# Performance work log

Hardware: AMD Instinct MI355X
Metric: run time of the kernel (lower is better)

The kernel has to match this reference:

```python
import jax, jax.numpy as jnp
import numpy as np

B, S, K, H = 512, 128, 4, 128  # batch, seq_len, interest_num, hidden_size
ROUTING_TIMES = 3
EPS = 1e-9


def setup_inputs() -> dict:
    key = jax.random.key(0)
    k1, k2 = jax.random.split(key)
    item_eb = jax.random.normal(k1, (B, S, H), dtype=jnp.float32)
    mask = jnp.ones((B, S), dtype=jnp.float32)
    # learned bilinear map parameter (bilinear_type == 2)
    w = jax.random.normal(k2, (1, S, K * H, H), dtype=jnp.float32) * 0.02
    return {"item_eb": item_eb, "mask": mask, "w": w}


def _squash(cap):
    # cap: [B, K, 1, H]
    n = jnp.sum(cap * cap, axis=-1, keepdims=True)
    return (n / (1.0 + n) / jnp.sqrt(n + EPS)) * cap


def reference(item_eb, mask, w):
    # bilinear_type==2: sum(w[:, :S] * item_eb[:, :, None, :], axis=3)
    # expressed as an einsum to avoid the [B,S,K*H,H] intermediate
    item_eb_hat = jnp.einsum('bsh,sdh->bsd', item_eb, w[0])          # [B, S, K*H]
    item_eb_hat = item_eb_hat.reshape(B, S, K, H).transpose(0, 2, 1, 3)  # [B, K, S, H]
    hat_iter = jax.lax.stop_gradient(item_eb_hat)  # stop_grad=True

    atten_mask = jnp.broadcast_to(mask[:, None, :], (B, K, S))
    capsule_weight = jnp.zeros((B, K, S), dtype=item_eb.dtype)  # bilinear_type > 0

    interest_capsule = None
    for i in range(ROUTING_TIMES):
        # torch F.softmax with implicit dim on a 3D tensor -> dim=0 (legacy)
        sw = jax.nn.softmax(capsule_weight, axis=0)
        sw = jnp.where(atten_mask == 0, 0.0, sw)[:, :, None, :]  # [B, K, 1, S]
        src = hat_iter if i < 2 else item_eb_hat
        interest_capsule = _squash(jnp.matmul(sw, src))  # [B, K, 1, H]
        if i < 2:
            delta = jnp.matmul(hat_iter, interest_capsule.transpose(0, 1, 3, 2))  # [B,K,S,1]
            capsule_weight = capsule_weight + delta.reshape(B, K, S)

    return interest_capsule.reshape(B, K, H)
```

## Files before the change

### kernel.cpp

```cpp
#include <hip/hip_runtime.h>
#include <math.h>

#define BB 512
#define SS 128
#define KK 4
#define HH 128
#define DD 512

typedef __attribute__((ext_vector_type(8))) short bf16x8;
typedef __attribute__((ext_vector_type(4))) float f32x4;

__device__ __forceinline__ unsigned short f2bf(float f) {
  unsigned u = __float_as_uint(f);
  unsigned r = u + 0x7fffu + ((u >> 16) & 1u);
  return (unsigned short)(r >> 16);
}
__device__ __forceinline__ ushort4 f2bf4(float4 v) {
  ushort4 o; o.x = f2bf(v.x); o.y = f2bf(v.y); o.z = f2bf(v.z); o.w = f2bf(v.w);
  return o;
}
__device__ __forceinline__ float bfhi(unsigned u) { return __uint_as_float(u & 0xffff0000u); }
__device__ __forceinline__ float bflo(unsigned u) { return __uint_as_float(u << 16); }

__global__ __launch_bounds__(256) void einsum_mfma(
    const float* __restrict__ item,
    const float* __restrict__ w,
    unsigned short* __restrict__ hat)
{
  __shared__ unsigned short Al[128 * 128];
  __shared__ unsigned short Wl[2][128 * 64];
  const int s  = blockIdx.x;
  const int b0 = blockIdx.y * 128;
  const int t  = threadIdx.x;
  const int lane = t & 63, wvq = t >> 6;
  const int qm = wvq & 1, qn = wvq >> 1;
  const int n16 = lane & 15, kq = lane >> 4;

  const float* Abase = item + ((size_t)b0 * SS + s) * HH;
  const float* Wbase = w + (size_t)s * DD * HH;

  const int ac = t & 31, ar0 = t >> 5;
  const int wc = t & 15, wr0 = t >> 4;
  float4 apre[16];
  #pragma unroll
  for (int j = 0; j < 16; ++j)
    apre[j] = *(const float4*)(Abase + (size_t)(ar0 + 8 * j) * (SS * HH) + ac * 4);
  float4 wpre[8];
  #pragma unroll
  for (int j = 0; j < 8; ++j)
    wpre[j] = *(const float4*)(Wbase + (size_t)(wr0 + 16 * j) * HH + wc * 4);

  #pragma unroll
  for (int j = 0; j < 16; ++j) {
    const int r = ar0 + 8 * j;
    const int lg = ac >> 1;
    *(ushort4*)&Al[r * 128 + ((lg ^ (r & 15)) * 8) + (ac & 1) * 4] = f2bf4(apre[j]);
  }
  #pragma unroll
  for (int j = 0; j < 8; ++j) {
    const int r = wr0 + 16 * j;
    *(ushort4*)&Wl[0][r * 64 + ((((wc >> 1) + r) & 7) * 8) + (wc & 1) * 4] = f2bf4(wpre[j]);
  }
  __syncthreads();

  int buf = 0;
  for (int dt = 0; dt < 4; ++dt) {
    f32x4 acc[4][4] = {};
    #pragma unroll
    for (int hs = 0; hs < 2; ++hs) {
      const int step = dt * 2 + hs;
      if (step < 7) {
        const int d0n = ((step + 1) >> 1) * 128;
        const int ksn = ((step + 1) & 1) * 64;
        #pragma unroll
        for (int j = 0; j < 8; ++j)
          wpre[j] = *(const float4*)(Wbase + (size_t)(d0n + wr0 + 16 * j) * HH + ksn + wc * 4);
      }
      #pragma unroll
      for (int kk = 0; kk < 2; ++kk) {
        bf16x8 af[4], bfr[4];
        #pragma unroll
        for (int i = 0; i < 4; ++i) {
          const int ra = qm * 64 + i * 16 + n16;
          const int rb = qn * 64 + i * 16 + n16;
          af[i]  = *(const bf16x8*)&Wl[buf][ra * 64 + ((kk * 4 + kq + ra) & 7) * 8];
          bfr[i] = *(const bf16x8*)&Al[rb * 128 + (((hs * 8 + kk * 4 + kq) ^ (rb & 15)) * 8)];
        }
        #pragma unroll
        for (int i = 0; i < 4; ++i)
          #pragma unroll
          for (int j = 0; j < 4; ++j)
            acc[i][j] = __builtin_amdgcn_mfma_f32_16x16x32_bf16(af[i], bfr[j], acc[i][j], 0, 0, 0);
      }
      if (step < 7) {
        #pragma unroll
        for (int j = 0; j < 8; ++j) {
          const int r = wr0 + 16 * j;
          *(ushort4*)&Wl[buf ^ 1][r * 64 + ((((wc >> 1) + r) & 7) * 8) + (wc & 1) * 4] = f2bf4(wpre[j]);
        }
        __syncthreads();
        buf ^= 1;
      }
    }
    #pragma unroll
    for (int j = 0; j < 4; ++j) {
      const int b = b0 + qn * 64 + j * 16 + n16;
      unsigned short* orow = hat + (((size_t)b * KK + dt) * SS + s) * HH;
      #pragma unroll
      for (int i = 0; i < 4; ++i) {
        const int h = qm * 64 + i * 16 + kq * 4;
        ushort4 o;
        o.x = f2bf(acc[i][j][0]); o.y = f2bf(acc[i][j][1]);
        o.z = f2bf(acc[i][j][2]); o.w = f2bf(acc[i][j][3]);
        *(ushort4*)(orow + h) = o;
      }
    }
  }
}

__global__ __launch_bounds__(256) void softmax_k(
    const float* __restrict__ cw, const float* __restrict__ mask,
    float* __restrict__ sw)
{
  __shared__ float rbuf[4];
  const int s = blockIdx.x, k = blockIdx.y, t = threadIdx.x;
  const size_t base = ((size_t)k * SS + s) * BB;
  float v0 = cw[base + t], v1 = cw[base + 256 + t];
  float m = fmaxf(v0, v1);
  #pragma unroll
  for (int o = 32; o; o >>= 1) m = fmaxf(m, __shfl_xor(m, o));
  if ((t & 63) == 0) rbuf[t >> 6] = m;
  __syncthreads();
  m = fmaxf(fmaxf(rbuf[0], rbuf[1]), fmaxf(rbuf[2], rbuf[3]));
  float e0 = expf(v0 - m), e1 = expf(v1 - m);
  float ssum = e0 + e1;
  #pragma unroll
  for (int o = 32; o; o >>= 1) ssum += __shfl_xor(ssum, o);
  __syncthreads();
  if ((t & 63) == 0) rbuf[t >> 6] = ssum;
  __syncthreads();
  float inv = 1.f / (rbuf[0] + rbuf[1] + rbuf[2] + rbuf[3]);
  float m0 = mask[(size_t)t * SS + s];
  float m1 = mask[(size_t)(t + 256) * SS + s];
  sw[base + t]       = (m0 == 0.f) ? 0.f : e0 * inv;
  sw[base + 256 + t] = (m1 == 0.f) ? 0.f : e1 * inv;
}

__global__ __launch_bounds__(256) void routing_k(
    const unsigned short* __restrict__ hat, const float* __restrict__ mask,
    const float* __restrict__ sw_in, float* __restrict__ cw,
    float* __restrict__ out, int mode)
{
  __shared__ float sw_l[128];
  __shared__ float4 red4[8][32];
  __shared__ float4 cq4[32];
  const int b = blockIdx.x, k = blockIdx.y, t = threadIdx.x;

  if (t < 128) {
    sw_l[t] = (mode == 0)
      ? ((mask[(size_t)b * SS + t] == 0.f) ? 0.f : (1.f / 512.f))
      : sw_in[((size_t)k * SS + t) * BB + b];
  }
  __syncthreads();

  const unsigned short* slab = hat + ((size_t)b * KK + k) * SS * HH;

  {
    const int h4 = t & 31, sg = t >> 5;
    float4 a = make_float4(0.f, 0.f, 0.f, 0.f);
    #pragma unroll
    for (int i = 0; i < 16; i++) {
      const int sr = sg * 16 + i;
      uint2 v = *(const uint2*)(slab + (size_t)sr * HH + h4 * 4);
      float ww = sw_l[sr];
      a.x = fmaf(ww, bflo(v.x), a.x);
      a.y = fmaf(ww, bfhi(v.x), a.y);
      a.z = fmaf(ww, bflo(v.y), a.z);
      a.w = fmaf(ww, bfhi(v.y), a.w);
    }
    red4[sg][h4] = a;
  }
  __syncthreads();

  if (t < 32) {
    float4 cap = red4[0][t];
    #pragma unroll
    for (int sg = 1; sg < 8; sg++) {
      float4 r = red4[sg][t];
      cap.x += r.x; cap.y += r.y; cap.z += r.z; cap.w += r.w;
    }
    float sq = cap.x * cap.x + cap.y * cap.y + cap.z * cap.z + cap.w * cap.w;
    #pragma unroll
    for (int o = 16; o; o >>= 1) sq += __shfl_xor(sq, o);
    const float n = sq;
    const float fac = n / (1.f + n) / sqrtf(n + 1e-9f);
    cap.x *= fac; cap.y *= fac; cap.z *= fac; cap.w *= fac;
    cq4[t] = cap;
    if (mode == 2)
      ((float4*)(out + ((size_t)b * KK + k) * HH))[t] = cap;
  }

  if (mode < 2) {
    __syncthreads();
    const int sr = t >> 1, hh = t & 1;
    const uint4* rowp = (const uint4*)(slab + (size_t)sr * HH + hh * 64);
    float d = 0.f;
    #pragma unroll
    for (int j = 0; j < 8; j++) {
      uint4 v = rowp[j];
      float4 qa = cq4[hh * 16 + 2 * j];
      float4 qb = cq4[hh * 16 + 2 * j + 1];
      d += bflo(v.x) * qa.x + bfhi(v.x) * qa.y
         + bflo(v.y) * qa.z + bfhi(v.y) * qa.w
         + bflo(v.z) * qb.x + bfhi(v.z) * qb.y
         + bflo(v.w) * qb.z + bfhi(v.w) * qb.w;
    }
    d += __shfl_xor(d, 1);
    if (hh == 0) {
      float* p = cw + ((size_t)k * SS + sr) * BB + b;
      if (mode == 0) *p = d; else *p += d;
    }
  }
}

extern "C" void kernel_launch(void* const* d_in, const int* in_sizes, int n_in,
                              void* d_out, int out_size, void* d_ws, size_t ws_size,
                              hipStream_t stream) {
  const float* item_eb = (const float*)d_in[0];
  const float* mask    = (const float*)d_in[1];
  const float* w       = (const float*)d_in[2];
  float* out = (float*)d_out;

  char* ws = (char*)d_ws;
  unsigned short* hat_bf = (unsigned short*)ws;
  float* cw  = (float*)(ws + 67108864);
  float* swb = (float*)(ws + 68157440);

  einsum_mfma<<<dim3(128, 4), 256, 0, stream>>>(item_eb, w, hat_bf);

  routing_k<<<dim3(BB, KK), 256, 0, stream>>>(hat_bf, mask, nullptr, cw, out, 0);
  softmax_k<<<dim3(SS, KK), 256, 0, stream>>>(cw, mask, swb);
  routing_k<<<dim3(BB, KK), 256, 0, stream>>>(hat_bf, mask, swb, cw, out, 1);
  softmax_k<<<dim3(SS, KK), 256, 0, stream>>>(cw, mask, swb);
  routing_k<<<dim3(BB, KK), 256, 0, stream>>>(hat_bf, mask, swb, cw, out, 2);
}
```

Baseline: 185.2 us.

## Hold each hat slab in registers with one wave per routing block

The routing kernel now runs one 64-thread wave per (b,k). Each lane loads its two hidden columns for all 128 sequence rows into 128 registers, so the slab is read from global memory once and reused for both the capsule sum and the delta dot product. The softmax output is transposed to a [B,K,S] layout so the routing kernel can read it contiguously. The cost is very high register pressure per thread, possibly spilling, far fewer threads per block, and an LDS transpose-reduce done in four chunks with barriers.

```diff
diff --git a/kernel.cpp b/kernel.cpp
--- a/kernel.cpp
+++ b/kernel.cpp
@@ -119,7 +119,8 @@
 }
 
 __global__ __launch_bounds__(256) void softmax_k(
-    const float* __restrict__ cw, const float* __restrict__ mask,
+    const float* __restrict__ cw,
+    const float* __restrict__ mask,
     float* __restrict__ sw)
 {
   __shared__ float rbuf[4];
@@ -142,84 +143,73 @@
   float inv = 1.f / (rbuf[0] + rbuf[1] + rbuf[2] + rbuf[3]);
   float m0 = mask[(size_t)t * SS + s];
   float m1 = mask[(size_t)(t + 256) * SS + s];
-  sw[base + t]       = (m0 == 0.f) ? 0.f : e0 * inv;
-  sw[base + 256 + t] = (m1 == 0.f) ? 0.f : e1 * inv;
-}
-
-__global__ __launch_bounds__(256) void routing_k(
-    const unsigned short* __restrict__ hat, const float* __restrict__ mask,
-    const float* __restrict__ sw_in, float* __restrict__ cw,
+  sw[(size_t)t * (KK * SS) + k * SS + s]         = (m0 == 0.f) ? 0.f : e0 * inv;
+  sw[(size_t)(t + 256) * (KK * SS) + k * SS + s] = (m1 == 0.f) ? 0.f : e1 * inv;
+}
+
+__global__ __launch_bounds__(64, 2) void routing_k(
+    const unsigned short* __restrict__ hat,
+    const float* __restrict__ mask,
+    const float* __restrict__ sw_in,
+    float* __restrict__ cw,
     float* __restrict__ out, int mode)
 {
   __shared__ float sw_l[128];
-  __shared__ float4 red4[8][32];
-  __shared__ float4 cq4[32];
-  const int b = blockIdx.x, k = blockIdx.y, t = threadIdx.x;
-
-  if (t < 128) {
-    sw_l[t] = (mode == 0)
-      ? ((mask[(size_t)b * SS + t] == 0.f) ? 0.f : (1.f / 512.f))
-      : sw_in[((size_t)k * SS + t) * BB + b];
-  }
-  __syncthreads();
-
-  const unsigned short* slab = hat + ((size_t)b * KK + k) * SS * HH;
-
-  {
-    const int h4 = t & 31, sg = t >> 5;
-    float4 a = make_float4(0.f, 0.f, 0.f, 0.f);
-    #pragma unroll
-    for (int i = 0; i < 16; i++) {
-      const int sr = sg * 16 + i;
-      uint2 v = *(const uint2*)(slab + (size_t)sr * HH + h4 * 4);
-      float ww = sw_l[sr];
-      a.x = fmaf(ww, bflo(v.x), a.x);
-      a.y = fmaf(ww, bfhi(v.x), a.y);
-      a.z = fmaf(ww, bflo(v.y), a.z);
-      a.w = fmaf(ww, bfhi(v.y), a.w);
-    }
-    red4[sg][h4] = a;
-  }
-  __syncthreads();
-
-  if (t < 32) {
-    float4 cap = red4[0][t];
-    #pragma unroll
-    for (int sg = 1; sg < 8; sg++) {
-      float4 r = red4[sg][t];
-      cap.x += r.x; cap.y += r.y; cap.z += r.z; cap.w += r.w;
-    }
-    float sq = cap.x * cap.x + cap.y * cap.y + cap.z * cap.z + cap.w * cap.w;
-    #pragma unroll
-    for (int o = 16; o; o >>= 1) sq += __shfl_xor(sq, o);
-    const float n = sq;
-    const float fac = n / (1.f + n) / sqrtf(n + 1e-9f);
-    cap.x *= fac; cap.y *= fac; cap.z *= fac; cap.w *= fac;
-    cq4[t] = cap;
-    if (mode == 2)
-      ((float4*)(out + ((size_t)b * KK + k) * HH))[t] = cap;
-  }
-
-  if (mode < 2) {
+  __shared__ float red[32][65];
+  const int b = blockIdx.x, k = blockIdx.y;
+  const int l = threadIdx.x;
+
+  const unsigned* slab = (const unsigned*)(hat + ((size_t)(b * KK + k) * SS) * HH);
+  unsigned hp[128];
+  #pragma unroll
+  for (int s = 0; s < 128; ++s) hp[s] = slab[s * 64 + l];
+
+  if (mode == 0) {
+    float2 mv = ((const float2*)(mask + (size_t)b * SS))[l];
+    sw_l[2 * l]     = (mv.x == 0.f) ? 0.f : (1.f / 512.f);
+    sw_l[2 * l + 1] = (mv.y == 0.f) ? 0.f : (1.f / 512.f);
+  } else {
+    float2 sv = ((const float2*)(sw_in + ((size_t)b * KK + k) * SS))[l];
+    sw_l[2 * l] = sv.x; sw_l[2 * l + 1] = sv.y;
+  }
+  __syncthreads();
+
+  float c0 = 0.f, c1 = 0.f;
+  #pragma unroll
+  for (int s = 0; s < 128; ++s) {
+    float wv = sw_l[s];
+    c0 = fmaf(wv, bflo(hp[s]), c0);
+    c1 = fmaf(wv, bfhi(hp[s]), c1);
+  }
+  float sq = c0 * c0 + c1 * c1;
+  #pragma unroll
+  for (int o = 32; o; o >>= 1) sq += __shfl_xor(sq, o);
+  const float fac = sq / (1.f + sq) / sqrtf(sq + 1e-9f);
+  c0 *= fac; c1 *= fac;
+
+  if (mode == 2) {
+    ((float2*)(out + ((size_t)b * KK + k) * HH))[l] = make_float2(c0, c1);
+    return;
+  }
+
+  #pragma unroll
+  for (int c = 0; c < 4; ++c) {
+    #pragma unroll
+    for (int j = 0; j < 32; ++j) {
+      const int s = c * 32 + j;
+      red[j][l] = fmaf(bflo(hp[s]), c0, bfhi(hp[s]) * c1);
+    }
     __syncthreads();
-    const int sr = t >> 1, hh = t & 1;
-    const uint4* rowp = (const uint4*)(slab + (size_t)sr * HH + hh * 64);
-    float d = 0.f;
-    #pragma unroll
-    for (int j = 0; j < 8; j++) {
-      uint4 v = rowp[j];
-      float4 qa = cq4[hh * 16 + 2 * j];
-      float4 qb = cq4[hh * 16 + 2 * j + 1];
-      d += bflo(v.x) * qa.x + bfhi(v.x) * qa.y
-         + bflo(v.y) * qa.z + bfhi(v.y) * qa.w
-         + bflo(v.z) * qb.x + bfhi(v.z) * qb.y
-         + bflo(v.w) * qb.z + bfhi(v.w) * qb.w;
-    }
-    d += __shfl_xor(d, 1);
-    if (hh == 0) {
-      float* p = cw + ((size_t)k * SS + sr) * BB + b;
-      if (mode == 0) *p = d; else *p += d;
-    }
+    const int sp = l >> 1, half = l & 1;
+    float dsum = 0.f;
+    #pragma unroll
+    for (int q = 0; q < 32; ++q) dsum += red[sp][half * 32 + q];
+    dsum += __shfl_xor(dsum, 1);
+    if (half == 0) {
+      float* p = cw + ((size_t)k * SS + c * 32 + sp) * BB + b;
+      if (mode == 0) *p = dsum; else *p += dsum;
+    }
+    __syncthreads();
   }
 }
 
@@ -238,9 +228,9 @@
 
   einsum_mfma<<<dim3(128, 4), 256, 0, stream>>>(item_eb, w, hat_bf);
 
-  routing_k<<<dim3(BB, KK), 256, 0, stream>>>(hat_bf, mask, nullptr, cw, out, 0);
+  routing_k<<<dim3(BB, KK), 64, 0, stream>>>(hat_bf, mask, nullptr, cw, out, 0);
   softmax_k<<<dim3(SS, KK), 256, 0, stream>>>(cw, mask, swb);
-  routing_k<<<dim3(BB, KK), 256, 0, stream>>>(hat_bf, mask, swb, cw, out, 1);
+  routing_k<<<dim3(BB, KK), 64, 0, stream>>>(hat_bf, mask, swb, cw, out, 1);
   softmax_k<<<dim3(SS, KK), 256, 0, stream>>>(cw, mask, swb);
-  routing_k<<<dim3(BB, KK), 256, 0, stream>>>(hat_bf, mask, swb, cw, out, 2);
-}
+  routing_k<<<dim3(BB, KK), 64, 0, stream>>>(hat_bf, mask, swb, cw, out, 2);
+}
```

Result: slower. 194.5 us (+5.1%).
